# Performance work log

Measured on AMD Instinct MI355X. Metric: run time of the kernel, lower is better.

The kernel has to match this reference:

```python
import jax, jax.numpy as jnp
import numpy as np

B, S, D, H = 4, 2048, 1024, 16
HD = D // H

def setup_inputs() -> dict:
    key = jax.random.key(0)
    ks = jax.random.split(key, 10)
    s = 1.0 / np.sqrt(D)
    inp = {
        'x': jax.random.normal(ks[0], (B, S, D), dtype=jnp.float32),
        'attention_mask': jnp.ones((B, S), dtype=jnp.int32),
        'Wq': jax.random.uniform(ks[1], (D, D), jnp.float32, -s, s),
        'bq': jax.random.uniform(ks[2], (D,), jnp.float32, -s, s),
        'Wk': jax.random.uniform(ks[3], (D, D), jnp.float32, -s, s),
        'bk': jax.random.uniform(ks[4], (D,), jnp.float32, -s, s),
        'Wv': jax.random.uniform(ks[5], (D, D), jnp.float32, -s, s),
        'bv': jax.random.uniform(ks[6], (D,), jnp.float32, -s, s),
        'Wo': jax.random.uniform(ks[7], (D, D), jnp.float32, -s, s),
        'bo': jax.random.uniform(ks[8], (D,), jnp.float32, -s, s),
    }
    return inp

def reference(x, Wq, bq, Wk, bk, Wv, bv, Wo, bo, attention_mask):
    scale = HD ** -0.5
    # torch Linear: y = x @ W^T + b
    def proj(W, b):
        return (x @ W.T + b).reshape(B, S, H, HD).transpose(0, 2, 1, 3)  # [B,H,S,hd]
    q = proj(Wq, bq)
    k = proj(Wk, bk)
    v = proj(Wv, bv)
    scores = jnp.einsum('bhqd,bhkd->bhqk', q, k) * scale  # [B,H,S,S]
    causal = jnp.triu(jnp.ones((S, S), dtype=bool), k=1)
    scores = jnp.where(causal, -jnp.inf, scores)
    pad = (attention_mask == 0)[:, None, None, :]  # [B,1,1,S]
    scores = jnp.where(pad, jnp.float32(-1e9), scores)
    probs = jax.nn.softmax(scores, axis=-1)
    out = jnp.einsum('bhqk,bhkd->bhqd', probs, v)  # [B,H,S,hd]
    out = out.transpose(0, 2, 1, 3).reshape(B, S, D)
    return out @ Wo.T + bo
```

## Files before the change

### kernel.cpp

```cpp
#include <hip/hip_runtime.h>
#include <hip/hip_bf16.h>

typedef unsigned short u16;
typedef float f32x4 __attribute__((ext_vector_type(4)));
typedef __bf16 bf16x8 __attribute__((ext_vector_type(8)));

#define BB 4
#define SS 2048
#define DD 1024
#define HH 16
#define HDD 64
#define MM (BB*SS)

__device__ __forceinline__ u16 f2bf(float f){
    union { float f; unsigned int i; } v; v.f = f;
    unsigned int i = v.i;
    return (u16)((i + 0x7FFFu + ((i >> 16) & 1u)) >> 16);
}
__device__ __forceinline__ ushort2 pk2(float a, float b){
    union { __hip_bfloat162 h; ushort2 u; } v;
    float2 t; t.x = a; t.y = b;
    v.h = __float22bfloat162_rn(t);
    return v.u;
}
__device__ __forceinline__ ushort4 pk4(float a, float b, float c, float d){
    ushort2 lo = pk2(a, b), hi = pk2(c, d);
    ushort4 r; r.x = lo.x; r.y = lo.y; r.z = hi.x; r.w = hi.y;
    return r;
}
__device__ __forceinline__ void gl2lds16(const void* g, void* l){
    __builtin_amdgcn_global_load_lds(
        (const __attribute__((address_space(1))) void*)g,
        (__attribute__((address_space(3))) void*)l, 16, 0, 0);
}

__device__ __forceinline__ void cvt8(const float* __restrict__ src,
                                     u16* __restrict__ dst, size_t i)
{
    const float4 a = *(const float4*)&src[i];
    const float4 b = *(const float4*)&src[i + 4];
    ushort4 lo = pk4(a.x, a.y, a.z, a.w);
    ushort4 hi = pk4(b.x, b.y, b.z, b.w);
    uint4 o;
    o.x = (unsigned)lo.x | ((unsigned)lo.y << 16);
    o.y = (unsigned)lo.z | ((unsigned)lo.w << 16);
    o.z = (unsigned)hi.x | ((unsigned)hi.y << 16);
    o.w = (unsigned)hi.z | ((unsigned)hi.w << 16);
    *(uint4*)&dst[i] = o;
}

__global__ __launch_bounds__(256) void cvt_k(const float* __restrict__ src,
                                             u16* __restrict__ dst)
{
    const size_t i = ((size_t)blockIdx.x * 256 + threadIdx.x) * 8;
    cvt8(src, dst, i);
}

__global__ __launch_bounds__(256) void cvtw3_k(
    const float* __restrict__ W0, const float* __restrict__ W1,
    const float* __restrict__ W2, u16* __restrict__ dst)
{
    const float* src = blockIdx.y == 0 ? W0 : (blockIdx.y == 1 ? W1 : W2);
    u16* d = dst + (size_t)blockIdx.y * (size_t)DD * DD;
    const size_t i = ((size_t)blockIdx.x * 256 + threadIdx.x) * 8;
    cvt8(src, d, i);
}

__global__ __launch_bounds__(256) void cvtw1_k(const float* __restrict__ W,
                                               u16* __restrict__ dst)
{
    const size_t i = ((size_t)blockIdx.x * 256 + threadIdx.x) * 8;
    cvt8(W, dst, i);
}

__device__ __forceinline__ void gemm_core(const u16* __restrict__ A,
                                          const u16* __restrict__ Wb,
                                          f32x4 (&acc)[4][4],
                                          u16* At, u16* Bt,
                                          int m0, int n0, int tid)
{
    const int lane = tid & 63, w = tid >> 6;
    const int quad = lane >> 4, l15 = lane & 15;
    const int wm = w >> 1, wn = w & 1;
    const int arow = lane >> 2;
    const int acol = (lane & 3) * 8;

    for (int k0 = 0; k0 < DD; k0 += 64) {
        __syncthreads();
        #pragma unroll
        for (int s = 0; s < 2; ++s) {
            #pragma unroll
            for (int c = 0; c < 2; ++c) {
                const int ch = w * 2 + c;
                gl2lds16(&A[(size_t)(m0 + ch * 16 + arow) * DD + k0 + s * 32 + acol],
                         &At[s * 4096 + ch * 512]);
                gl2lds16(&Wb[(size_t)(n0 + ch * 16 + arow) * DD + k0 + s * 32 + acol],
                         &Bt[s * 4096 + ch * 512]);
            }
        }
        __syncthreads();
        #pragma unroll
        for (int s = 0; s < 2; ++s) {
            bf16x8 af[4], bfr[4];
            #pragma unroll
            for (int i = 0; i < 4; ++i)
                af[i] = *(const bf16x8*)&At[s * 4096 + (wm * 64 + i * 16 + l15) * 32 + quad * 8];
            #pragma unroll
            for (int j = 0; j < 4; ++j)
                bfr[j] = *(const bf16x8*)&Bt[s * 4096 + (wn * 64 + j * 16 + l15) * 32 + quad * 8];
            #pragma unroll
            for (int i = 0; i < 4; ++i)
                #pragma unroll
                for (int j = 0; j < 4; ++j)
                    acc[i][j] = __builtin_amdgcn_mfma_f32_16x16x32_bf16(af[i], bfr[j], acc[i][j], 0, 0, 0);
        }
    }
}

__global__ __launch_bounds__(256, 4) void gemm_qkv_k(
    const u16* __restrict__ x,
    const float* __restrict__ bq, const float* __restrict__ bk,
    const float* __restrict__ bv,
    const u16* __restrict__ Wqb, const u16* __restrict__ Wkb,
    const u16* __restrict__ Wvb,
    u16* __restrict__ Q, u16* __restrict__ K, u16* __restrict__ V)
{
    __shared__ alignas(16) u16 At[128 * 64];
    __shared__ alignas(16) u16 Bt[128 * 64];
    const int tid = threadIdx.x, lane = tid & 63, w = tid >> 6;
    const int quad = lane >> 4, l15 = lane & 15;
    const int wm = w >> 1, wn = w & 1;
    const int z = blockIdx.z;
    const u16* Wmb = z == 0 ? Wqb : (z == 1 ? Wkb : Wvb);
    const float* bias = z == 0 ? bq : (z == 1 ? bk : bv);
    u16* Out = z == 0 ? Q : (z == 1 ? K : V);
    const int m0 = blockIdx.x * 128, n0 = blockIdx.y * 128;

    f32x4 acc[4][4];
    #pragma unroll
    for (int i = 0; i < 4; ++i)
        #pragma unroll
        for (int j = 0; j < 4; ++j) acc[i][j] = (f32x4)(0.0f);

    gemm_core(x, Wmb, acc, At, Bt, m0, n0, tid);

    float bs[4];
    #pragma unroll
    for (int j = 0; j < 4; ++j) bs[j] = bias[n0 + wn * 64 + j * 16 + l15];

    const int b = m0 / SS;
    const int h = (n0 + wn * 64) / HDD;
    const size_t base = ((size_t)(b * HH + h)) * SS * HDD;
    #pragma unroll
    for (int i = 0; i < 4; ++i) {
        #pragma unroll
        for (int r = 0; r < 4; ++r) {
            const int s = (m0 % SS) + wm * 64 + i * 16 + quad * 4 + r;
            #pragma unroll
            for (int j = 0; j < 4; ++j) {
                const int hd = j * 16 + l15;
                Out[base + (size_t)s * HDD + hd] = f2bf(acc[i][j][r] + bs[j]);
            }
        }
    }
}

__global__ __launch_bounds__(256, 4) void gemm_out_k(
    const u16* __restrict__ A, const float* __restrict__ bo,
    const u16* __restrict__ Wob, float* __restrict__ Out)
{
    __shared__ alignas(16) u16 At[128 * 64];
    __shared__ alignas(16) u16 Bt[128 * 64];
    const int tid = threadIdx.x, lane = tid & 63, w = tid >> 6;
    const int quad = lane >> 4, l15 = lane & 15;
    const int wm = w >> 1, wn = w & 1;
    const int m0 = blockIdx.x * 128, n0 = blockIdx.y * 128;

    f32x4 acc[4][4];
    #pragma unroll
    for (int i = 0; i < 4; ++i)
        #pragma unroll
        for (int j = 0; j < 4; ++j) acc[i][j] = (f32x4)(0.0f);

    gemm_core(A, Wob, acc, At, Bt, m0, n0, tid);

    float bs[4];
    #pragma unroll
    for (int j = 0; j < 4; ++j) bs[j] = bo[n0 + wn * 64 + j * 16 + l15];

    #pragma unroll
    for (int i = 0; i < 4; ++i) {
        #pragma unroll
        for (int r = 0; r < 4; ++r) {
            const int m = m0 + wm * 64 + i * 16 + quad * 4 + r;
            #pragma unroll
            for (int j = 0; j < 4; ++j) {
                const int n = n0 + wn * 64 + j * 16 + l15;
                Out[(size_t)m * DD + n] = acc[i][j][r] + bs[j];
            }
        }
    }
}

#define QT 256
#define KT 64
#define LDPV 66

#define LOG2E 1.4426950408889634f

__device__ __forceinline__ int swz128(int row, int bcol){
    return row * 128 + (bcol ^ ((row & 7) << 4));
}

__global__ __launch_bounds__(512, 3) void attn_k(
    const u16* __restrict__ Q, const u16* __restrict__ K,
    const u16* __restrict__ V, const int* __restrict__ mask,
    u16* __restrict__ AO)
{
    __shared__ alignas(16) u16 QPs[QT * 64];
    __shared__ alignas(16) u16 Ks[KT * 64];
    __shared__ alignas(16) u16 Vs[HDD * LDPV];
    __shared__ float padf[KT];

    const int tid = threadIdx.x, lane = tid & 63, w = tid >> 6;
    const int quad = lane >> 4, l15 = lane & 15;
    const int bh = blockIdx.x;
    const int y = blockIdx.y;
    const int qt = (y < 4) ? (7 - y) : (y - 4);
    const int b = bh >> 4, h = bh & 15;
    const int q0 = qt * QT;
    const size_t hoff = (size_t)bh * SS * HDD;
    const u16* Qh = Q + hoff;
    const u16* Kh = K + hoff;
    const u16* Vh = V + hoff;
    const int nkt = (q0 + QT) / KT;
    const float scale2 = 0.125f * LOG2E;
    const int wrow_end = q0 + w * 32 + 32;

    const int kslot = w * 64 + lane;
    const int krow = kslot >> 3;
    const int kbcol = ((kslot & 7) << 4) ^ ((krow & 7) << 4);

    for (int c = tid; c < QT * 8; c += 512) {
        const int row = c >> 3, cc = c & 7;
        *(uint4*)((char*)QPs + swz128(row, cc * 16)) =
            *(const uint4*)&Qh[(size_t)(q0 + row) * HDD + cc * 8];
    }
    __syncthreads();

    bf16x8 bQ[2][2];
    #pragma unroll
    for (int j = 0; j < 2; ++j)
        #pragma unroll
        for (int ks = 0; ks < 2; ++ks)
            bQ[j][ks] = *(const bf16x8*)((const char*)QPs +
                swz128(w * 32 + j * 16 + l15, ks * 64 + quad * 16));

    float m_run[2] = { -1e30f, -1e30f };
    float l_run[2] = { 0.f, 0.f };
    f32x4 o[4][2];
    #pragma unroll
    for (int i = 0; i < 4; ++i)
        #pragma unroll
        for (int j = 0; j < 2; ++j) o[i][j] = (f32x4)(0.0f);

    for (int kt = 0; kt < nkt; ++kt) {
        const int kt0 = kt * KT;
        __syncthreads();

        gl2lds16((const char*)Kh + (size_t)(kt0 + krow) * 128 + kbcol,
                 (char*)Ks + w * 1024);

        if (tid < 256) {
            const int kp = tid >> 3;
            const int c0 = (tid & 7) * 8;
            uint4 r0 = *(const uint4*)&Vh[(size_t)(kt0 + kp * 2 + 0) * HDD + c0];
            uint4 r1 = *(const uint4*)&Vh[(size_t)(kt0 + kp * 2 + 1) * HDD + c0];
            const u16* e0 = (const u16*)&r0;
            const u16* e1 = (const u16*)&r1;
            #pragma unroll
            for (int e = 0; e < 8; ++e) {
                ushort2 pkv; pkv.x = e0[e]; pkv.y = e1[e];
                *(ushort2*)&Vs[(c0 + e) * LDPV + kp * 2] = pkv;
            }
        } else if (tid < 320) {
            const int t = tid - 256;
            padf[t] = (mask[b * SS + kt0 + t] == 0) ? -1e9f : 0.0f;
        }
        __syncthreads();

        if (kt0 < wrow_end) {
        f32x4 sc[4][2];
        #pragma unroll
        for (int i = 0; i < 4; ++i)
            #pragma unroll
            for (int j = 0; j < 2; ++j) sc[i][j] = (f32x4)(0.0f);
        __builtin_amdgcn_s_setprio(1);
        #pragma unroll
        for (int ks = 0; ks < 2; ++ks) {
            bf16x8 aK[4];
            #pragma unroll
            for (int i = 0; i < 4; ++i)
                aK[i] = *(const bf16x8*)((const char*)Ks +
                    swz128(i * 16 + l15, ks * 64 + quad * 16));
            #pragma unroll
            for (int i = 0; i < 4; ++i)
                #pragma unroll
                for (int j = 0; j < 2; ++j)
                    sc[i][j] = __builtin_amdgcn_mfma_f32_16x16x32_bf16(aK[i], bQ[j][ks], sc[i][j], 0, 0, 0);
        }
        __builtin_amdgcn_s_setprio(0);

        f32x4 pb[4];
        #pragma unroll
        for (int i = 0; i < 4; ++i)
            pb[i] = *(const f32x4*)&padf[i * 16 + quad * 4];

        #pragma unroll
        for (int j = 0; j < 2; ++j) {
            const int qrow = q0 + w * 32 + j * 16 + l15;
            const bool needC = (kt0 + KT - 1) > (q0 + w * 32 + j * 16);
            float mx = -1e9f;
            if (needC) {
                #pragma unroll
                for (int i = 0; i < 4; ++i)
                    #pragma unroll
                    for (int r = 0; r < 4; ++r) {
                        const int kpg = kt0 + i * 16 + quad * 4 + r;
                        float s = fmaf(sc[i][j][r], scale2, pb[i][r]);
                        s = (kpg > qrow) ? -1e9f : s;
                        sc[i][j][r] = s; mx = fmaxf(mx, s);
                    }
            } else {
                #pragma unroll
                for (int i = 0; i < 4; ++i)
                    #pragma unroll
                    for (int r = 0; r < 4; ++r) {
                        float s = fmaf(sc[i][j][r], scale2, pb[i][r]);
                        sc[i][j][r] = s; mx = fmaxf(mx, s);
                    }
            }
            mx = fmaxf(mx, __shfl_xor(mx, 16, 64));
            mx = fmaxf(mx, __shfl_xor(mx, 32, 64));
            float nm = m_run[j];
            if (!__all(mx <= nm + 8.f)) {
                nm = fmaxf(nm, mx);
                const float alpha = __builtin_exp2f(m_run[j] - nm);
                m_run[j] = nm;
                l_run[j] *= alpha;
                #pragma unroll
                for (int i = 0; i < 4; ++i)
                    #pragma unroll
                    for (int r = 0; r < 4; ++r) o[i][j][r] *= alpha;
            }
            float rs = 0.f;
            #pragma unroll
            for (int i = 0; i < 4; ++i) {
                float p0 = __builtin_exp2f(sc[i][j][0] - nm);
                float p1 = __builtin_exp2f(sc[i][j][1] - nm);
                float p2 = __builtin_exp2f(sc[i][j][2] - nm);
                float p3 = __builtin_exp2f(sc[i][j][3] - nm);
                rs += (p0 + p1) + (p2 + p3);
                *(ushort4*)((char*)QPs + swz128(w * 32 + j * 16 + l15, i * 32 + quad * 8)) =
                    pk4(p0, p1, p2, p3);
            }
            l_run[j] += rs;
        }
        asm volatile("s_waitcnt lgkmcnt(0)" ::: "memory");

        __builtin_amdgcn_s_setprio(1);
        #pragma unroll
        for (int ks = 0; ks < 2; ++ks) {
            bf16x8 aV[4], bP[2];
            #pragma unroll
            for (int i = 0; i < 4; ++i)
                aV[i] = *(const bf16x8*)&Vs[(i * 16 + l15) * LDPV + ks * 32 + quad * 8];
            #pragma unroll
            for (int j = 0; j < 2; ++j)
                bP[j] = *(const bf16x8*)((const char*)QPs +
                    swz128(w * 32 + j * 16 + l15, ks * 64 + quad * 16));
            #pragma unroll
            for (int i = 0; i < 4; ++i)
                #pragma unroll
                for (int j = 0; j < 2; ++j)
                    o[i][j] = __builtin_amdgcn_mfma_f32_16x16x32_bf16(aV[i], bP[j], o[i][j], 0, 0, 0);
        }
        __builtin_amdgcn_s_setprio(0);
        }
    }

    #pragma unroll
    for (int j = 0; j < 2; ++j) {
        float l = l_run[j];
        l += __shfl_xor(l, 16, 64);
        l += __shfl_xor(l, 32, 64);
        const float inv = (l > 0.f) ? (1.f / l) : 0.f;
        const int s = q0 + w * 32 + j * 16 + l15;
        const size_t rb = ((size_t)(b * SS + s)) * DD + h * HDD;
        #pragma unroll
        for (int i = 0; i < 4; ++i)
            *(ushort4*)&AO[rb + i * 16 + quad * 4] =
                pk4(o[i][j][0] * inv, o[i][j][1] * inv, o[i][j][2] * inv, o[i][j][3] * inv);
    }
}

extern "C" void kernel_launch(void* const* d_in, const int* in_sizes, int n_in,
                              void* d_out, int out_size, void* d_ws, size_t ws_size,
                              hipStream_t stream)
{
    const float* x  = (const float*)d_in[0];
    const int* mask = (const int*)d_in[1];
    const float* Wq = (const float*)d_in[2];
    const float* bq = (const float*)d_in[3];
    const float* Wk = (const float*)d_in[4];
    const float* bk = (const float*)d_in[5];
    const float* Wv = (const float*)d_in[6];
    const float* bv = (const float*)d_in[7];
    const float* Wo = (const float*)d_in[8];
    const float* bo = (const float*)d_in[9];
    float* out = (float*)d_out;

    u16* ws = (u16*)d_ws;
    const size_t NE = (size_t)MM * DD;
    const size_t WE = (size_t)DD * DD;
    if (ws_size < 4 * NE * sizeof(u16)) return;

    u16* Qb = ws;
    u16* Kb = ws + NE;
    u16* Vb = ws + 2 * NE;
    u16* Ab = ws + 3 * NE;

    u16* Wscr = (u16*)d_out;

    dim3 blk(256);
    cvt_k<<<dim3(NE / 2048), blk, 0, stream>>>(x, Ab);
    cvtw3_k<<<dim3(WE / 2048, 3), blk, 0, stream>>>(Wq, Wk, Wv, Wscr);
    gemm_qkv_k<<<dim3(MM / 128, DD / 128, 3), blk, 0, stream>>>(
        Ab, bq, bk, bv, Wscr, Wscr + WE, Wscr + 2 * WE, Qb, Kb, Vb);
    attn_k<<<dim3(BB * HH, SS / QT), dim3(512), 0, stream>>>(Qb, Kb, Vb, mask, Ab);
    cvtw1_k<<<dim3(WE / 2048), blk, 0, stream>>>(Wo, Qb);
    gemm_out_k<<<dim3(MM / 128, DD / 128), blk, 0, stream>>>(Ab, bo, Qb, out);
}
```

Measured before the change: 305.7 us.

## Double-buffer GEMM LDS tiles and remap blocks for XCD-local L2 reuse

Splits the GEMM's 64-wide K step into two 32-wide halves held in ping-pong LDS buffers. The async global-to-LDS load for the next half is issued before computing the current one, so load latency overlaps MFMA work and only one barrier is needed per half-step. Both GEMMs now use a 1D grid with a swizzle that places consecutive M tiles of the same N column on the same XCD, improving L2 reuse of shared A/B rows. The unroll-1 loop and tighter barrier placement may reduce ILP, and correctness depends on the async copy completing before the next barrier.

```diff
diff --git a/kernel.cpp b/kernel.cpp
--- a/kernel.cpp
+++ b/kernel.cpp
@@ -76,7 +76,8 @@
 __device__ __forceinline__ void gemm_core(const u16* __restrict__ A,
                                           const u16* __restrict__ Wb,
                                           f32x4 (&acc)[4][4],
-                                          u16* At, u16* Bt,
+                                          u16 (&At)[2][128 * 32],
+                                          u16 (&Bt)[2][128 * 32],
                                           int m0, int n0, int tid)
 {
     const int lane = tid & 63, w = tid >> 6;
@@ -85,36 +86,51 @@
     const int arow = lane >> 2;
     const int acol = (lane & 3) * 8;
 
-    for (int k0 = 0; k0 < DD; k0 += 64) {
+    auto STG = [&](int bi, int kt) {
+        const int kk = kt * 32;
+        #pragma unroll
+        for (int c = 0; c < 2; ++c) {
+            const int ch = w * 2 + c;
+            gl2lds16(&A [(size_t)(m0 + ch * 16 + arow) * DD + kk + acol], &At[bi][ch * 512]);
+            gl2lds16(&Wb[(size_t)(n0 + ch * 16 + arow) * DD + kk + acol], &Bt[bi][ch * 512]);
+        }
+    };
+    auto CMP = [&](int bi) {
+        bf16x8 af[4], bfr[4];
+        #pragma unroll
+        for (int i = 0; i < 4; ++i)
+            af[i] = *(const bf16x8*)&At[bi][(wm * 64 + i * 16 + l15) * 32 + quad * 8];
+        #pragma unroll
+        for (int j = 0; j < 4; ++j)
+            bfr[j] = *(const bf16x8*)&Bt[bi][(wn * 64 + j * 16 + l15) * 32 + quad * 8];
+        #pragma unroll
+        for (int i = 0; i < 4; ++i)
+            #pragma unroll
+            for (int j = 0; j < 4; ++j)
+                acc[i][j] = __builtin_amdgcn_mfma_f32_16x16x32_bf16(af[i], bfr[j], acc[i][j], 0, 0, 0);
+    };
+
+    STG(0, 0);
+    __syncthreads();
+    #pragma unroll 1
+    for (int i = 0; i < 15; ++i) {
+        STG(1, 2 * i + 1);
+        CMP(0);
         __syncthreads();
-        #pragma unroll
-        for (int s = 0; s < 2; ++s) {
-            #pragma unroll
-            for (int c = 0; c < 2; ++c) {
-                const int ch = w * 2 + c;
-                gl2lds16(&A[(size_t)(m0 + ch * 16 + arow) * DD + k0 + s * 32 + acol],
-                         &At[s * 4096 + ch * 512]);
-                gl2lds16(&Wb[(size_t)(n0 + ch * 16 + arow) * DD + k0 + s * 32 + acol],
-                         &Bt[s * 4096 + ch * 512]);
-            }
-        }
+        STG(0, 2 * i + 2);
+        CMP(1);
         __syncthreads();
-        #pragma unroll
-        for (int s = 0; s < 2; ++s) {
-            bf16x8 af[4], bfr[4];
-            #pragma unroll
-            for (int i = 0; i < 4; ++i)
-                af[i] = *(const bf16x8*)&At[s * 4096 + (wm * 64 + i * 16 + l15) * 32 + quad * 8];
-            #pragma unroll
-            for (int j = 0; j < 4; ++j)
-                bfr[j] = *(const bf16x8*)&Bt[s * 4096 + (wn * 64 + j * 16 + l15) * 32 + quad * 8];
-            #pragma unroll
-            for (int i = 0; i < 4; ++i)
-                #pragma unroll
-                for (int j = 0; j < 4; ++j)
-                    acc[i][j] = __builtin_amdgcn_mfma_f32_16x16x32_bf16(af[i], bfr[j], acc[i][j], 0, 0, 0);
-        }
-    }
+    }
+    STG(1, 31);
+    CMP(0);
+    __syncthreads();
+    CMP(1);
+}
+
+__device__ __forceinline__ void xcd_map(int bid, int& m0, int& n0){
+    const int xcd = bid & 7, q = bid >> 3;
+    m0 = (xcd * 8 + (q & 7)) * 128;
+    n0 = (q >> 3) * 128;
 }
 
 __global__ __launch_bounds__(256, 4) void gemm_qkv_k(
@@ -125,16 +141,17 @@
     const u16* __restrict__ Wvb,
     u16* __restrict__ Q, u16* __restrict__ K, u16* __restrict__ V)
 {
-    __shared__ alignas(16) u16 At[128 * 64];
-    __shared__ alignas(16) u16 Bt[128 * 64];
+    __shared__ alignas(16) u16 At[2][128 * 32];
+    __shared__ alignas(16) u16 Bt[2][128 * 32];
     const int tid = threadIdx.x, lane = tid & 63, w = tid >> 6;
     const int quad = lane >> 4, l15 = lane & 15;
     const int wm = w >> 1, wn = w & 1;
-    const int z = blockIdx.z;
+    const int z = blockIdx.y;
     const u16* Wmb = z == 0 ? Wqb : (z == 1 ? Wkb : Wvb);
     const float* bias = z == 0 ? bq : (z == 1 ? bk : bv);
     u16* Out = z == 0 ? Q : (z == 1 ? K : V);
-    const int m0 = blockIdx.x * 128, n0 = blockIdx.y * 128;
+    int m0, n0;
+    xcd_map(blockIdx.x, m0, n0);
 
     f32x4 acc[4][4];
     #pragma unroll
@@ -169,12 +186,13 @@
     const u16* __restrict__ A, const float* __restrict__ bo,
     const u16* __restrict__ Wob, float* __restrict__ Out)
 {
-    __shared__ alignas(16) u16 At[128 * 64];
-    __shared__ alignas(16) u16 Bt[128 * 64];
+    __shared__ alignas(16) u16 At[2][128 * 32];
+    __shared__ alignas(16) u16 Bt[2][128 * 32];
     const int tid = threadIdx.x, lane = tid & 63, w = tid >> 6;
     const int quad = lane >> 4, l15 = lane & 15;
     const int wm = w >> 1, wn = w & 1;
-    const int m0 = blockIdx.x * 128, n0 = blockIdx.y * 128;
+    int m0, n0;
+    xcd_map(blockIdx.x, m0, n0);
 
     f32x4 acc[4][4];
     #pragma unroll
@@ -435,9 +453,9 @@
     dim3 blk(256);
     cvt_k<<<dim3(NE / 2048), blk, 0, stream>>>(x, Ab);
     cvtw3_k<<<dim3(WE / 2048, 3), blk, 0, stream>>>(Wq, Wk, Wv, Wscr);
-    gemm_qkv_k<<<dim3(MM / 128, DD / 128, 3), blk, 0, stream>>>(
+    gemm_qkv_k<<<dim3(512, 3), blk, 0, stream>>>(
         Ab, bq, bk, bv, Wscr, Wscr + WE, Wscr + 2 * WE, Qb, Kb, Vb);
     attn_k<<<dim3(BB * HH, SS / QT), dim3(512), 0, stream>>>(Qb, Kb, Vb, mask, Ab);
     cvtw1_k<<<dim3(WE / 2048), blk, 0, stream>>>(Wo, Qb);
-    gemm_out_k<<<dim3(MM / 128, DD / 128), blk, 0, stream>>>(Ab, bo, Qb, out);
-}
+    gemm_out_k<<<dim3(512), blk, 0, stream>>>(Ab, bo, Qb, out);
+}
```

New measurement: 315.9 us. +3.3%, slower.
